# Kernel optimization log

Hardware: AMD Instinct MI355X
Metric: run time of the kernel (lower is better)

The kernel has to match this reference:

```python
import jax, jax.numpy as jnp
import numpy as np

H, W = 512, 512
CHUNK = 128            # gaussians blended per scan step
BLUR = 0.3             # antialiasing dilation (as in 3DGS EWA low-pass)
ALPHA_MIN = 1.0 / 255.0
ALPHA_MAX = 0.99


def setup_inputs() -> dict:
    key = jax.random.key(0)
    k = jax.random.split(key, 6)
    N = 8192
    means2D = jax.random.uniform(k[0], (N, 2), jnp.float32) * jnp.array([W, H], jnp.float32)
    colors = jax.random.uniform(k[1], (N, 3), jnp.float32)
    opacities = jax.random.uniform(k[2], (N, 1), jnp.float32)
    scales = jax.random.uniform(k[3], (N, 2), jnp.float32) * 15.0 + 1.0   # pixels
    rotations = jax.random.uniform(k[4], (N, 1), jnp.float32) * (2.0 * np.pi)
    depths = jax.random.uniform(k[5], (N,), jnp.float32)
    background = jnp.zeros((3,), jnp.float32)
    return dict(means2D=means2D, colors=colors, opacities=opacities,
                scales=scales, rotations=rotations, depths=depths,
                background=background)


def _rasterize(means2D, colors, opacities, scales, rotations, depths, background):
    # depth sort: front (small depth) first
    order = jnp.argsort(depths)
    m = means2D[order]                 # [N,2] (x,y)
    col = colors[order]                # [N,3]
    op = opacities[order][:, 0]        # [N]
    s = scales[order]                  # [N,2]
    th = rotations[order][:, 0]        # [N]

    # 2D covariance  Sigma = R diag(s^2) R^T
    c, si = jnp.cos(th), jnp.sin(th)
    sx2, sy2 = s[:, 0] ** 2, s[:, 1] ** 2
    A = c * c * sx2 + si * si * sy2
    Cc = si * si * sx2 + c * c * sy2
    B = c * si * (sx2 - sy2)
    det = A * Cc - B * B
    # antialiasing: dilate covariance, compensate opacity
    A2, C2 = A + BLUR, Cc + BLUR
    det2 = A2 * C2 - B * B
    op = op * jnp.sqrt(jnp.maximum(det / det2, 0.0))
    invdet = 1.0 / det2
    ia, ib, ic = C2 * invdet, -B * invdet, A2 * invdet   # Sigma^-1 entries

    # pixel centers
    ys, xs = jnp.meshgrid(jnp.arange(H, dtype=jnp.float32) + 0.5,
                          jnp.arange(W, dtype=jnp.float32) + 0.5, indexing='ij')

    N = m.shape[0]
    nchunk = N // CHUNK
    chunk = lambda a: a.reshape((nchunk, CHUNK) + a.shape[1:])
    gs = (chunk(m), chunk(col), chunk(op), chunk(ia), chunk(ib), chunk(ic))

    def step(carry, g):
        T, acc = carry                       # T:[H,W] transmittance, acc:[3,H,W]
        gm, gcol, gop, gia, gib, gic = g     # per-chunk [C,...]
        dx = xs[None] - gm[:, 0, None, None]                 # [C,H,W]
        dy = ys[None] - gm[:, 1, None, None]
        power = (-0.5 * (gia[:, None, None] * dx * dx + gic[:, None, None] * dy * dy)
                 - gib[:, None, None] * dx * dy)
        alpha = jnp.minimum(ALPHA_MAX, gop[:, None, None] * jnp.exp(power))
        alpha = jnp.where(alpha < ALPHA_MIN, 0.0, alpha)     # skip tiny splats (as CUDA)
        one_m = 1.0 - alpha
        cum = jnp.cumprod(one_m, axis=0)                     # inclusive
        Twithin = jnp.concatenate([jnp.ones_like(cum[:1]), cum[:-1]], 0)  # exclusive
        w = alpha * Twithin * T[None]                        # blend weight per gaussian
        acc = acc + jnp.einsum('nc,nhw->chw', gcol, w)
        T = T * cum[-1]
        return (T, acc), None

    init = (jnp.ones((H, W), jnp.float32), jnp.zeros((3, H, W), jnp.float32))
    (T, acc), _ = jax.lax.scan(step, init, gs)
    color = acc + background[:, None, None] * T[None]        # [3,H,W]
    return color


def reference(means2D, colors, opacities, scales, rotations, depths, background):
    return _rasterize(means2D, colors, opacities, scales, rotations, depths, background)
```

## Files before the change

### kernel.cpp

```cpp
#include <hip/hip_runtime.h>
#include <stdint.h>

#define HH 512
#define WW 512
#define ALPHA_MIN_C (1.0f/255.0f)
#define ALPHA_MAX_C 0.99f
#define BLUR_C 0.3f
#define TERM_EPS 1.0e-4f

#define JCHUNK 1024
__global__ __launch_bounds__(256) void rank_kernel(const float* __restrict__ depths,
                                                   int N, int* __restrict__ rank) {
    __shared__ uint64_t sk[JCHUNK];
    const int tid = threadIdx.x;
    const int ngb = N >> 8;
    const int gb = blockIdx.x % ngb;
    const int jb = blockIdx.x / ngb;
    const int j0 = jb * JCHUNK;
    for (int i = tid; i < JCHUNK; i += 256) {
        int j = j0 + i;
        uint32_t bits = __float_as_uint(depths[j]);
        sk[i] = ((uint64_t)bits << 32) | (uint32_t)j;
    }
    __syncthreads();
    const int g = gb * 256 + tid;
    const uint32_t mb = __float_as_uint(depths[g]);
    const uint64_t mykey = ((uint64_t)mb << 32) | (uint32_t)g;
    int cnt = 0;
#pragma unroll 8
    for (int i = 0; i < JCHUNK; ++i)
        cnt += (sk[i] < mykey) ? 1 : 0;
    atomicAdd(&rank[g], cnt);
}

__global__ __launch_bounds__(256) void prep_kernel(
    const float* __restrict__ means, const float* __restrict__ colors,
    const float* __restrict__ ops, const float* __restrict__ scales,
    const float* __restrict__ rots, const int* __restrict__ rank, int N,
    float4* __restrict__ pA, float4* __restrict__ pB,
    float* __restrict__ pC, float* __restrict__ pR) {
    int g = blockIdx.x * 256 + threadIdx.x;
    if (g >= N) return;
    int pos = rank[g];
    float mx = means[2*g], my = means[2*g+1];
    float th = rots[g];
    float c = cosf(th), si = sinf(th);
    float sx = scales[2*g], sy = scales[2*g+1];
    float sx2 = sx*sx, sy2 = sy*sy;
    float A  = c*c*sx2 + si*si*sy2;
    float Cc = si*si*sx2 + c*c*sy2;
    float B  = c*si*(sx2 - sy2);
    float det = A*Cc - B*B;
    float A2 = A + BLUR_C, C2 = Cc + BLUR_C;
    float det2 = A2*C2 - B*B;
    float op = ops[g] * sqrtf(fmaxf(det/det2, 0.0f));
    float invd = 1.0f/det2;
    float ia = C2*invd, ib = -B*invd, ic = A2*invd;
    float mid = 0.5f*(A2+C2);
    float lam = mid + sqrtf(fmaxf(mid*mid - det2, 0.0f));
    float r2;
    if (op < ALPHA_MIN_C) {
        r2 = -1.0f;
    } else {
        float t = __logf(op * 255.0f);
        r2 = fmaxf(2.0f * lam * t, 0.0f) * 1.0001f + 0.25f;
    }
    pA[pos] = make_float4(mx, my, ia, ib);
    pB[pos] = make_float4(ic, op, colors[3*g], colors[3*g+1]);
    pC[pos] = colors[3*g+2];
    pR[pos] = r2;
}

__global__ __launch_bounds__(256) void blend_kernel(
    const float4* __restrict__ pA, const float4* __restrict__ pB,
    const float* __restrict__ pC, const float* __restrict__ pR,
    const float* __restrict__ bg, int N, float* __restrict__ out) {
    __shared__ float4 sA[256];
    __shared__ float4 sB[256];
    __shared__ float  sC[256];
    __shared__ int    wcnt[4];
    const int tid = threadIdx.x;
    const int tileX = blockIdx.x & 31, tileY = blockIdx.x >> 5;
    const int px = tileX*16 + (tid & 15);
    const int py = tileY*16 + (tid >> 4);
    const float fx = px + 0.5f, fy = py + 0.5f;
    const float x0 = tileX*16 + 0.5f, x1 = tileX*16 + 15.5f;
    const float y0 = tileY*16 + 0.5f, y1 = tileY*16 + 15.5f;
    const int lane = tid & 63, wid = tid >> 6;
    float T = 1.0f, accR = 0.0f, accG = 0.0f, accB = 0.0f;

    for (int base = 0; base < N; base += 256) {
        const int g = base + tid;
        float4 a = pA[g];
        float4 b = pB[g];
        float cb = pC[g];
        float r2 = pR[g];
        float nx = fminf(fmaxf(a.x, x0), x1) - a.x;
        float ny = fminf(fmaxf(a.y, y0), y1) - a.y;
        bool flag = (nx*nx + ny*ny) <= r2;
        uint64_t mask = __ballot(flag);
        if (lane == 0) wcnt[wid] = __popcll(mask);
        __syncthreads();
        int off = __popcll(mask & ((1ull << lane) - 1ull));
        for (int w2 = 0; w2 < wid; ++w2) off += wcnt[w2];
        const int M = wcnt[0] + wcnt[1] + wcnt[2] + wcnt[3];
        if (flag) { sA[off] = a; sB[off] = b; sC[off] = cb; }
        __syncthreads();
        for (int i = 0; i < M; ++i) {
            float4 ga = sA[i];
            float4 gb = sB[i];
            float dx = fx - ga.x, dy = fy - ga.y;
            float power = -0.5f*(ga.z*dx*dx + gb.x*dy*dy) - ga.w*dx*dy;
            float alpha = fminf(ALPHA_MAX_C, gb.y * __expf(power));
            if (alpha >= ALPHA_MIN_C) {
                float w = alpha * T;
                accR += gb.z * w;
                accG += gb.w * w;
                accB += sC[i] * w;
                T *= (1.0f - alpha);
            }
        }
        if (__syncthreads_and(T < TERM_EPS)) break;
    }
    const int pix = py*WW + px;
    out[pix]             = accR + bg[0]*T;
    out[pix +   HH*WW]   = accG + bg[1]*T;
    out[pix + 2*HH*WW]   = accB + bg[2]*T;
}

extern "C" void kernel_launch(void* const* d_in, const int* in_sizes, int n_in,
                              void* d_out, int out_size, void* d_ws, size_t ws_size,
                              hipStream_t stream) {
    const float* means   = (const float*)d_in[0];
    const float* colors  = (const float*)d_in[1];
    const float* ops     = (const float*)d_in[2];
    const float* scales  = (const float*)d_in[3];
    const float* rots    = (const float*)d_in[4];
    const float* depths  = (const float*)d_in[5];
    const float* bg      = (const float*)d_in[6];
    const int N = in_sizes[0] / 2;

    char* ws = (char*)d_ws;
    float4* pA  = (float4*)(ws);
    float4* pB  = (float4*)(ws + (size_t)N*16);
    float*  pC  = (float*)(ws + (size_t)N*32);
    float*  pR  = (float*)(ws + (size_t)N*36);
    int*    rank= (int*)  (ws + (size_t)N*40);

    hipMemsetAsync(rank, 0, (size_t)N*4, stream);

    const int ngb = N / 256;
    const int njb = N / JCHUNK;
    rank_kernel<<<dim3(ngb*njb), dim3(256), 0, stream>>>(depths, N, rank);
    prep_kernel<<<dim3((N+255)/256), dim3(256), 0, stream>>>(
        means, colors, ops, scales, rots, rank, N, pA, pB, pC, pR);
    blend_kernel<<<dim3((WW/16)*(HH/16)), dim3(256), 0, stream>>>(
        pA, pB, pC, pR, bg, N, (float*)d_out);
}
```

Before: 150.2 us.

## Use 8x8 wavefront subtiles with per-wave culling, prefetching, and 32-bit rank keys

```diff
diff --git a/kernel.cpp b/kernel.cpp
--- a/kernel.cpp
+++ b/kernel.cpp
@@ -8,28 +8,31 @@
 #define BLUR_C 0.3f
 #define TERM_EPS 1.0e-4f
 
-#define JCHUNK 1024
+#define JCHUNK 512
 __global__ __launch_bounds__(256) void rank_kernel(const float* __restrict__ depths,
                                                    int N, int* __restrict__ rank) {
-    __shared__ uint64_t sk[JCHUNK];
+    __shared__ uint32_t sk[JCHUNK];
     const int tid = threadIdx.x;
     const int ngb = N >> 8;
     const int gb = blockIdx.x % ngb;
-    const int jb = blockIdx.x / ngb;
-    const int j0 = jb * JCHUNK;
-    for (int i = tid; i < JCHUNK; i += 256) {
-        int j = j0 + i;
-        uint32_t bits = __float_as_uint(depths[j]);
-        sk[i] = ((uint64_t)bits << 32) | (uint32_t)j;
-    }
+    const int j0 = (blockIdx.x / ngb) * JCHUNK;
+    for (int i = tid; i < JCHUNK; i += 256)
+        sk[i] = __float_as_uint(depths[j0 + i]);
     __syncthreads();
     const int g = gb * 256 + tid;
     const uint32_t mb = __float_as_uint(depths[g]);
-    const uint64_t mykey = ((uint64_t)mb << 32) | (uint32_t)g;
+    const int glim = g - j0;
     int cnt = 0;
+    const uint4* sk4 = (const uint4*)sk;
 #pragma unroll 8
-    for (int i = 0; i < JCHUNK; ++i)
-        cnt += (sk[i] < mykey) ? 1 : 0;
+    for (int q = 0; q < JCHUNK / 4; ++q) {
+        uint4 v = sk4[q];
+        const int i4 = q * 4;
+        cnt += (v.x < mb) || (v.x == mb && (i4 + 0) < glim);
+        cnt += (v.y < mb) || (v.y == mb && (i4 + 1) < glim);
+        cnt += (v.z < mb) || (v.z == mb && (i4 + 2) < glim);
+        cnt += (v.w < mb) || (v.w == mb && (i4 + 3) < glim);
+    }
     atomicAdd(&rank[g], cnt);
 }
 
@@ -78,23 +81,28 @@
     __shared__ float4 sA[256];
     __shared__ float4 sB[256];
     __shared__ float  sC[256];
+    __shared__ float  sR[256];
     __shared__ int    wcnt[4];
     const int tid = threadIdx.x;
+    const int lane = tid & 63, wid = tid >> 6;
     const int tileX = blockIdx.x & 31, tileY = blockIdx.x >> 5;
-    const int px = tileX*16 + (tid & 15);
-    const int py = tileY*16 + (tid >> 4);
+    const int qx = tileX*16 + (wid & 1)*8;
+    const int qy = tileY*16 + (wid >> 1)*8;
+    const int px = qx + (lane & 7);
+    const int py = qy + (lane >> 3);
     const float fx = px + 0.5f, fy = py + 0.5f;
-    const float x0 = tileX*16 + 0.5f, x1 = tileX*16 + 15.5f;
-    const float y0 = tileY*16 + 0.5f, y1 = tileY*16 + 15.5f;
-    const int lane = tid & 63, wid = tid >> 6;
+    const float qx0 = qx + 0.5f, qx1 = qx + 7.5f;
+    const float qy0 = qy + 0.5f, qy1 = qy + 7.5f;
+    const float x0 = tileX*16 + 0.5f, x1 = x0 + 15.0f;
+    const float y0 = tileY*16 + 0.5f, y1 = y0 + 15.0f;
     float T = 1.0f, accR = 0.0f, accG = 0.0f, accB = 0.0f;
 
+    float4 a = pA[tid];
+    float4 b = pB[tid];
+    float cb = pC[tid];
+    float r2 = pR[tid];
+
     for (int base = 0; base < N; base += 256) {
-        const int g = base + tid;
-        float4 a = pA[g];
-        float4 b = pB[g];
-        float cb = pC[g];
-        float r2 = pR[g];
         float nx = fminf(fmaxf(a.x, x0), x1) - a.x;
         float ny = fminf(fmaxf(a.y, y0), y1) - a.y;
         bool flag = (nx*nx + ny*ny) <= r2;
@@ -104,20 +112,27 @@
         int off = __popcll(mask & ((1ull << lane) - 1ull));
         for (int w2 = 0; w2 < wid; ++w2) off += wcnt[w2];
         const int M = wcnt[0] + wcnt[1] + wcnt[2] + wcnt[3];
-        if (flag) { sA[off] = a; sB[off] = b; sC[off] = cb; }
+        if (flag) { sA[off] = a; sB[off] = b; sC[off] = cb; sR[off] = r2; }
         __syncthreads();
-        for (int i = 0; i < M; ++i) {
-            float4 ga = sA[i];
-            float4 gb = sB[i];
-            float dx = fx - ga.x, dy = fy - ga.y;
-            float power = -0.5f*(ga.z*dx*dx + gb.x*dy*dy) - ga.w*dx*dy;
-            float alpha = fminf(ALPHA_MAX_C, gb.y * __expf(power));
-            if (alpha >= ALPHA_MIN_C) {
-                float w = alpha * T;
-                accR += gb.z * w;
-                accG += gb.w * w;
-                accB += sC[i] * w;
-                T *= (1.0f - alpha);
+        const int gn = base + 256 + tid;
+        if (gn < N) { a = pA[gn]; b = pB[gn]; cb = pC[gn]; r2 = pR[gn]; }
+        if (!__all(T < TERM_EPS)) {
+            for (int i = 0; i < M; ++i) {
+                float4 ga = sA[i];
+                float wx = fminf(fmaxf(ga.x, qx0), qx1) - ga.x;
+                float wy = fminf(fmaxf(ga.y, qy0), qy1) - ga.y;
+                if (wx*wx + wy*wy > sR[i]) continue;
+                float4 gb = sB[i];
+                float dx = fx - ga.x, dy = fy - ga.y;
+                float power = -0.5f*(ga.z*dx*dx + gb.x*dy*dy) - ga.w*dx*dy;
+                float alpha = fminf(ALPHA_MAX_C, gb.y * __expf(power));
+                if (alpha >= ALPHA_MIN_C) {
+                    float w = alpha * T;
+                    accR += gb.z * w;
+                    accG += gb.w * w;
+                    accB += sC[i] * w;
+                    T *= (1.0f - alpha);
+                }
             }
         }
         if (__syncthreads_and(T < TERM_EPS)) break;
```

Measured after the change: 163.8 us. 1.09x slower.
